# Performance work log

Hardware: AMD Instinct MI355X
Metric: run time of the kernel (lower is better)

Reference implementation:

```python
import jax, jax.numpy as jnp
import numpy as np

BS, N, DIM, HEADS = 4, 2048, 512, 8
HEAD_DIM = DIM // HEADS
SCALE = HEAD_DIM ** 0.5
NEG = -1000000.0


def setup_inputs() -> dict:
    key = jax.random.key(0)
    ks = jax.random.split(key, 6)
    x = jax.random.normal(ks[0], (BS, N, DIM), dtype=jnp.float32)
    mask = jax.random.randint(ks[1], (BS, N), 0, 2, dtype=jnp.int32)
    s = 1.0 / np.sqrt(DIM)
    Wq = jax.random.normal(ks[2], (DIM, DIM), dtype=jnp.float32) * s
    Wk = jax.random.normal(ks[3], (DIM, DIM), dtype=jnp.float32) * s
    Wv = jax.random.normal(ks[4], (DIM, DIM), dtype=jnp.float32) * s
    Wo = jax.random.normal(ks[5], (DIM, DIM), dtype=jnp.float32) * s
    return {"x": x, "Wq": Wq, "Wk": Wk, "Wv": Wv, "Wo": Wo, "mask": mask}


def reference(x, Wq, Wk, Wv, Wo, mask):
    # q,k,v: (bs, n, dim) -> (bs, h, n, d)
    def split_heads(t):
        return t.reshape(BS, N, HEADS, HEAD_DIM).transpose(0, 2, 1, 3)
    q = split_heads(x @ Wq.T)
    k = split_heads(x @ Wk.T)
    v = split_heads(x @ Wv.T)
    # scores: (bs, h, n, n)
    scores = jnp.einsum('bhqd,bhkd->bhqk', q, k) / SCALE
    # key-padding mask broadcast over heads and query positions
    keep = (mask == 1)[:, None, None, :]  # (bs,1,1,n)
    scores = jnp.where(keep, scores, NEG)
    attn = jax.nn.softmax(scores, axis=-1)
    out = jnp.einsum('bhqk,bhkd->bhqd', attn, v)
    out = out.transpose(0, 2, 1, 3).reshape(BS, N, DIM)
    return out @ Wo.T
```

## Files before the change

### kernel.cpp

```cpp
#include <hip/hip_runtime.h>
#include <hip/hip_bf16.h>

#define BS 4
#define SEQ 2048
#define DIM 512
#define HEADS 8
#define HD 64
#define ROWS (BS*SEQ)
#define SCL2E 0.1803368801111244f
#define NEGB (-1.4426950408889634e6f)

typedef __attribute__((ext_vector_type(8))) short bf16x8;
typedef __attribute__((ext_vector_type(4))) short bf16x4;
typedef __attribute__((ext_vector_type(4))) float floatx4;
typedef unsigned short u16;
typedef unsigned int u32;

#if defined(__has_builtin)
# if __has_builtin(__builtin_amdgcn_mfma_f32_16x16x16bf16_1k)
#  define HAVE_MFMA16 1
# endif
#endif
#ifndef HAVE_MFMA16
# define HAVE_MFMA16 0
#endif

__device__ __forceinline__ u16 f2bf(float f) {
    union { float f; unsigned u; } v; v.f = f;
    unsigned r = v.u + 0x7fff + ((v.u >> 16) & 1);
    return (u16)(r >> 16);
}

__device__ __forceinline__ unsigned pack2bf(float a, float b) {
#if __has_builtin(__builtin_amdgcn_cvt_pk_bf16_f32)
    typedef __attribute__((ext_vector_type(2))) __bf16 bf2;
    union { bf2 v; unsigned u; } cv;
    cv.v = __builtin_amdgcn_cvt_pk_bf16_f32(a, b);
    return cv.u;
#else
    return (unsigned)f2bf(a) | ((unsigned)f2bf(b) << 16);
#endif
}

__device__ __forceinline__ float fexp2(float x) {
#if __has_builtin(__builtin_amdgcn_exp2f)
    return __builtin_amdgcn_exp2f(x);
#else
    return __expf(x * 0.6931471805599453f);
#endif
}

__device__ __forceinline__ void gload16(const u16* g, u16* l) {
    __builtin_amdgcn_global_load_lds(
        (const __attribute__((address_space(1))) u32*)g,
        (__attribute__((address_space(3))) u32*)l, 16, 0, 0);
}

__global__ __launch_bounds__(256) void convert_all(
    const float* __restrict__ x, const float* __restrict__ Wq,
    const float* __restrict__ Wk, const float* __restrict__ Wv,
    const float* __restrict__ Wo, const int* __restrict__ mask,
    u16* __restrict__ xb, u16* __restrict__ wqb,
    u16* __restrict__ wkb, u16* __restrict__ wvb,
    u16* __restrict__ wob, float* __restrict__ biasf)
{
    int i = blockIdx.x * 256 + threadIdx.x;
    if (i < 1048576 + 262144) {
        const float* src; u16* dst; int off;
        if (i < 1048576) { src = x; dst = xb; off = i; }
        else {
            int j = i - 1048576; int seg = j >> 16; off = j & 65535;
            src = seg == 0 ? Wq : seg == 1 ? Wk : seg == 2 ? Wv : Wo;
            dst = seg == 0 ? wqb : seg == 1 ? wkb : seg == 2 ? wvb : wob;
        }
        float4 v = ((const float4*)src)[off];
        ushort4 o;
        o.x = f2bf(v.x); o.y = f2bf(v.y); o.z = f2bf(v.z); o.w = f2bf(v.w);
        ((ushort4*)dst)[off] = o;
    } else {
        int jb = i - 1310720;
        int4 mv = ((const int4*)mask)[jb];
        float4 bo;
        bo.x = (mv.x == 1) ? 0.f : NEGB;
        bo.y = (mv.y == 1) ? 0.f : NEGB;
        bo.z = (mv.z == 1) ? 0.f : NEGB;
        bo.w = (mv.w == 1) ? 0.f : NEGB;
        ((float4*)biasf)[jb] = bo;
    }
}

__global__ __launch_bounds__(256, 3) void gemm_qkv_fused(
    const u16* __restrict__ A, const u16* __restrict__ Wcat,
    u16* __restrict__ Oq, u16* __restrict__ Okf, u16* __restrict__ Ovf)
{
    __shared__ u16 ldsA[8192];
    __shared__ u16 ldsB[8192];

    int n0 = blockIdx.x * 128;
    int m0 = blockIdx.y * 128;
    int tid = threadIdx.x;
    int w = tid >> 6, lane = tid & 63, quad = lane >> 4, l16 = lane & 15;
    int mo = (w & 1) * 64, no = (w >> 1) * 64;
    int l7 = l16 & 7;

    int sr = lane >> 3, sc = lane & 7, gc = sc ^ sr;
    const u16* gA0 = A    + (long)(m0 + sr) * DIM + gc * 8;
    const u16* gB0 = Wcat + (long)(n0 + sr) * DIM + gc * 8;

    floatx4 acc[4][4];
    #pragma unroll
    for (int mt = 0; mt < 4; mt++)
        #pragma unroll
        for (int nt = 0; nt < 4; nt++) acc[mt][nt] = (floatx4){0.f,0.f,0.f,0.f};

    for (int k0 = 0; k0 < DIM; k0 += 64) {
        #pragma unroll
        for (int i = 0; i < 4; i++) {
            int ch = w * 4 + i;
            gload16(gA0 + (long)ch * 8 * DIM + k0, &ldsA[ch * 512]);
            gload16(gB0 + (long)ch * 8 * DIM + k0, &ldsB[ch * 512]);
        }
        __syncthreads();

        #pragma unroll
        for (int kc = 0; kc < 2; kc++) {
            int swz = ((kc * 4 + quad) ^ l7) * 8;
            bf16x8 af[4], bf[4];
            #pragma unroll
            for (int t4 = 0; t4 < 4; t4++) {
                af[t4] = *(const bf16x8*)&ldsA[(mo + t4*16 + l16) * 64 + swz];
                bf[t4] = *(const bf16x8*)&ldsB[(no + t4*16 + l16) * 64 + swz];
            }
            #pragma unroll
            for (int mt = 0; mt < 4; mt++)
                #pragma unroll
                for (int nt = 0; nt < 4; nt++)
                    acc[mt][nt] = __builtin_amdgcn_mfma_f32_16x16x32_bf16(
                        af[mt], bf[nt], acc[mt][nt], 0, 0, 0);
        }
        __syncthreads();
    }

    int seg = n0 >> 9;
    if (seg == 0) {
        #pragma unroll
        for (int mt = 0; mt < 4; mt++)
            #pragma unroll
            for (int nt = 0; nt < 4; nt++)
                #pragma unroll
                for (int r = 0; r < 4; r++) {
                    int row = m0 + mo + mt*16 + quad*4 + r;
                    int col9 = (n0 + no + nt*16 + l16) & 511;
                    int b = row >> 11, n = row & 2047, h = col9 >> 6, d = col9 & 63;
                    Oq[(((long)(b * HEADS + h) * SEQ + n) << 6) + d] = f2bf(acc[mt][nt][r]);
                }
    } else if (seg == 1) {
        #pragma unroll
        for (int mt = 0; mt < 4; mt++)
            #pragma unroll
            for (int nt = 0; nt < 4; nt++)
                #pragma unroll
                for (int r = 0; r < 4; r++) {
                    int row = m0 + mo + mt*16 + quad*4 + r;
                    int col9 = (n0 + no + nt*16 + l16) & 511;
                    int b = row >> 11, keyn = row & 2047, h = col9 >> 6, dd = col9 & 63;
                    int kt = keyn >> 6, ntk = (keyn >> 4) & 3, l16k = keyn & 15;
                    int g = dd >> 5, quadk = (dd >> 3) & 3, j = dd & 7;
                    long offv = ((long)((b*HEADS + h)*32 + kt) << 12)
                              + ((ntk*2 + g) << 9) + ((quadk*16 + l16k) << 3) + j;
                    Okf[offv] = f2bf(acc[mt][nt][r] * SCL2E);
                }
    } else {
#if HAVE_MFMA16
        #pragma unroll
        for (int mt = 0; mt < 4; mt++)
            #pragma unroll
            for (int nt = 0; nt < 4; nt++) {
                int rowb = m0 + mo + mt*16 + quad*4;
                int col9 = (n0 + no + nt*16 + l16) & 511;
                int b = rowb >> 11, keyn = rowb & 2047, h = col9 >> 6, dd = col9 & 63;
                int kt = keyn >> 6;
                int wf = (keyn >> 4) & 3, quadf = (keyn >> 2) & 3;
                int ctf = dd >> 4, l16f = dd & 15;
                long offv = ((long)((b*HEADS + h)*32 + kt) << 12)
                          + (wf << 10) + ((quadf*16 + l16f) << 4) + (ctf << 2);
                ushort4 st;
                st.x = f2bf(acc[mt][nt][0]); st.y = f2bf(acc[mt][nt][1]);
                st.z = f2bf(acc[mt][nt][2]); st.w = f2bf(acc[mt][nt][3]);
                *(ushort4*)&Ovf[offv] = st;
            }
#else
        #pragma unroll
        for (int mt = 0; mt < 4; mt++)
            #pragma unroll
            for (int nt = 0; nt < 4; nt++) {
                int rowb = m0 + mo + mt*16 + quad*4;
                int col9 = (n0 + no + nt*16 + l16) & 511;
                int b = rowb >> 11, keyn = rowb & 2047, h = col9 >> 6, dd = col9 & 63;
                int kt = keyn >> 6, g = (keyn >> 5) & 1, quadv = (keyn >> 3) & 3, jk = keyn & 7;
                int ctv = dd >> 4, l16v = dd & 15;
                long offv = ((long)((b*HEADS + h)*32 + kt) << 12)
                          + ((ctv*2 + g) << 9) + ((quadv*16 + l16v) << 3) + jk;
                ushort4 st;
                st.x = f2bf(acc[mt][nt][0]); st.y = f2bf(acc[mt][nt][1]);
                st.z = f2bf(acc[mt][nt][2]); st.w = f2bf(acc[mt][nt][3]);
                *(ushort4*)&Ovf[offv] = st;
            }
#endif
    }
}

#if HAVE_MFMA16
__global__ __launch_bounds__(256, 3) void flash_attn(
    const u16* __restrict__ Q, const u16* __restrict__ Kf,
    const u16* __restrict__ Vf, const float* __restrict__ biasf,
    u16* __restrict__ ctx)
{
    __shared__ float red[4352];

    int bx = blockIdx.x;
    int q0 = (bx & 31) * 64;
    int h  = (bx >> 5) & 7;
    int b  = bx >> 8;
    int bh = b * HEADS + h;

    int tid = threadIdx.x;
    int w = tid >> 6, lane = tid & 63, quad = lane >> 4, l16 = lane & 15;

    bf16x8 qb[4][2];
    #pragma unroll
    for (int nt = 0; nt < 4; nt++) {
        const u16* qp = Q + ((long)bh * SEQ + q0 + nt*16 + l16) * HD + quad * 8;
        qb[nt][0] = *(const bf16x8*)(qp);
        qb[nt][1] = *(const bf16x8*)(qp + 32);
    }

    const u16* Kbh = Kf + ((long)bh << 17) + w*1024 + lane*8;
    const u16* Vbh = Vf + ((long)bh << 17) + w*1024 + lane*16;
    const float* bb = biasf + b * SEQ + w*16 + quad*4;

    bf16x8 ka0 = *(const bf16x8*)(Kbh);
    bf16x8 ka1 = *(const bf16x8*)(Kbh + 512);
    bf16x8 vlo = *(const bf16x8*)(Vbh);
    bf16x8 vhi = *(const bf16x8*)(Vbh + 8);
    float4 bv  = *(const float4*)(bb);

    floatx4 o[4][4];
    #pragma unroll
    for (int nt = 0; nt < 4; nt++)
        #pragma unroll
        for (int ct = 0; ct < 4; ct++) o[nt][ct] = (floatx4){0.f,0.f,0.f,0.f};
    float ls[4] = {0.f, 0.f, 0.f, 0.f};

    #pragma unroll 2
    for (int t = 0; t < 32; t++) {
        bf16x8 ka0n = ka0, ka1n = ka1, vlon = vlo, vhin = vhi;
        float4 bvn = bv;
        if (t < 31) {
            const u16* kp = Kbh + (long)(t+1)*4096;
            const u16* vp = Vbh + (long)(t+1)*4096;
            ka0n = *(const bf16x8*)(kp);
            ka1n = *(const bf16x8*)(kp + 512);
            vlon = *(const bf16x8*)(vp);
            vhin = *(const bf16x8*)(vp + 8);
            bvn  = *(const float4*)(bb + (t+1)*64);
        }

        union { bf16x8 v8; bf16x4 v4[2]; } uvl, uvh;
        uvl.v8 = vlo; uvh.v8 = vhi;
        bf16x4 vb[4] = { uvl.v4[0], uvl.v4[1], uvh.v4[0], uvh.v4[1] };

        #pragma unroll
        for (int nt = 0; nt < 4; nt++) {
            floatx4 s;
            s[0] = bv.x; s[1] = bv.y; s[2] = bv.z; s[3] = bv.w;
            s = __builtin_amdgcn_mfma_f32_16x16x32_bf16(ka0, qb[nt][0], s, 0, 0, 0);
            s = __builtin_amdgcn_mfma_f32_16x16x32_bf16(ka1, qb[nt][1], s, 0, 0, 0);
            float p0 = fexp2(s[0]);
            float p1 = fexp2(s[1]);
            float p2 = fexp2(s[2]);
            float p3 = fexp2(s[3]);
            ls[nt] += (p0 + p1) + (p2 + p3);
            union { bf16x4 v; unsigned u[2]; } pu;
            pu.u[0] = pack2bf(p0, p1);
            pu.u[1] = pack2bf(p2, p3);
            #pragma unroll
            for (int ct = 0; ct < 4; ct++)
                o[nt][ct] = __builtin_amdgcn_mfma_f32_16x16x16bf16_1k(
                    pu.v, vb[ct], o[nt][ct], 0, 0, 0);
        }

        ka0 = ka0n; ka1 = ka1n; vlo = vlon; vhi = vhin; bv = bvn;
    }

    __syncthreads();
    float* ldsf = red;
    floatx4* ldsv = (floatx4*)red;

    #pragma unroll
    for (int nt = 0; nt < 4; nt++) {
        ls[nt] += __shfl_xor(ls[nt], 16);
        ls[nt] += __shfl_xor(ls[nt], 32);
    }
    if (quad == 0) {
        #pragma unroll
        for (int nt = 0; nt < 4; nt++)
            ldsf[4096 + w*64 + nt*16 + l16] = ls[nt];
    }
    __syncthreads();

    #pragma unroll
    for (int i = 1; i < 4; i++) {
        int tslot = (w + i) & 3;
        #pragma unroll
        for (int nt = 0; nt < 4; nt++)
            if (nt == tslot) {
                #pragma unroll
                for (int ct = 0; ct < 4; ct++)
                    ldsv[nt*256 + ct*64 + lane] = o[nt][ct];
            }
        __syncthreads();
        #pragma unroll
        for (int nt = 0; nt < 4; nt++)
            if (nt == w) {
                #pragma unroll
                for (int ct = 0; ct < 4; ct++) {
                    floatx4 v = ldsv[nt*256 + ct*64 + lane];
                    o[nt][ct] += v;
                }
            }
        __syncthreads();
    }

    #pragma unroll
    for (int nt = 0; nt < 4; nt++) {
        if (nt != w) continue;
        float inv[4];
        #pragma unroll
        for (int r = 0; r < 4; r++) {
            int q = w*16 + quad*4 + r;
            float s = ldsf[4096 + q] + ldsf[4096 + 64 + q]
                    + ldsf[4096 + 128 + q] + ldsf[4096 + 192 + q];
            inv[r] = 1.0f / s;
        }
        #pragma unroll
        for (int ct = 0; ct < 4; ct++) {
            int col = h * HD + ct*16 + l16;
            long rb = (long)(b * SEQ + q0 + w*16 + quad*4);
            #pragma unroll
            for (int r = 0; r < 4; r++)
                ctx[(rb + r) * DIM + col] = f2bf(o[nt][ct][r] * inv[r]);
        }
    }
}
#else
__global__ __launch_bounds__(256, 4) void flash_attn(
    const u16* __restrict__ Q, const u16* __restrict__ Kf,
    const u16* __restrict__ Vf, const float* __restrict__ biasf,
    u16* __restrict__ ctx)
{
    __shared__ u16 lds[20480];

    int bx = blockIdx.x;
    int q0 = (bx & 31) * 64;
    int h  = (bx >> 5) & 7;
    int b  = bx >> 8;
    int bh = b * HEADS + h;

    int tid = threadIdx.x;
    int w = tid >> 6, lane = tid & 63, quad = lane >> 4, l16 = lane & 15;

    const u16* Qp = Q + ((long)bh * SEQ + q0 + w*16 + l16) * HD + quad * 8;
    bf16x8 qb0 = *(const bf16x8*)(Qp);
    bf16x8 qb1 = *(const bf16x8*)(Qp + 32);

    const u16* Kbh = Kf + ((long)bh << 17);
    const u16* Vbh = Vf + ((long)bh << 17);
    const float* bbase = biasf + b * SEQ + quad * 4;

    u16* Prow = &lds[16384 + w * 1024 + l16 * 64];
    int swz = l16 & 7;

    {
        const u16* gk = Kbh + (2*w)*512 + lane*8;
        const u16* gv = Vbh + (2*w)*512 + lane*8;
        gload16(gk,       &lds[(2*w)*512]);
        gload16(gk + 512, &lds[(2*w+1)*512]);
        gload16(gv,       &lds[8192 + (2*w)*512]);
        gload16(gv + 512, &lds[8192 + (2*w+1)*512]);
    }
    __syncthreads();

    floatx4 o[4];
    #pragma unroll
    for (int ct = 0; ct < 4; ct++) o[ct] = (floatx4){0.f, 0.f, 0.f, 0.f};
    float lsum = 0.f;

    for (int t = 0; t < 32; t++) {
        int cur = t & 1;
        if (t < 31) {
            long tb = (long)(t + 1) << 12;
            int nb = cur ^ 1;
            const u16* gk = Kbh + tb + (2*w)*512 + lane*8;
            const u16* gv = Vbh + tb + (2*w)*512 + lane*8;
            gload16(gk,       &lds[nb*4096 + (2*w)*512]);
            gload16(gk + 512, &lds[nb*4096 + (2*w+1)*512]);
            gload16(gv,       &lds[8192 + nb*4096 + (2*w)*512]);
            gload16(gv + 512, &lds[8192 + nb*4096 + (2*w+1)*512]);
        }

        const u16* Kl = &lds[cur * 4096];
        const u16* Vl = &lds[8192 + cur * 4096];

        #pragma unroll
        for (int nt = 0; nt < 4; nt++) {
            float4 bv = *(const float4*)(bbase + t*64 + nt*16);
            bf16x8 ka0 = *(const bf16x8*)(Kl + (nt*2 + 0)*512 + lane*8);
            bf16x8 ka1 = *(const bf16x8*)(Kl + (nt*2 + 1)*512 + lane*8);
            floatx4 tt;
            tt[0] = bv.x; tt[1] = bv.y; tt[2] = bv.z; tt[3] = bv.w;
            tt = __builtin_amdgcn_mfma_f32_16x16x32_bf16(ka0, qb0, tt, 0, 0, 0);
            tt = __builtin_amdgcn_mfma_f32_16x16x32_bf16(ka1, qb1, tt, 0, 0, 0);
            float p0 = fexp2(tt[0]);
            float p1 = fexp2(tt[1]);
            float p2 = fexp2(tt[2]);
            float p3 = fexp2(tt[3]);
            lsum += (p0 + p1) + (p2 + p3);
            int gx = nt*2 + (quad >> 1);
            uint2 pu;
            pu.x = pack2bf(p0, p1);
            pu.y = pack2bf(p2, p3);
            *(uint2*)(Prow + ((gx ^ swz) << 3) + (quad & 1)*4) = pu;
        }

        #pragma unroll
        for (int g = 0; g < 2; g++) {
            bf16x8 pa = *(const bf16x8*)(Prow + (((g*4 + quad) ^ swz) << 3));
            #pragma unroll
            for (int ct = 0; ct < 4; ct++) {
                bf16x8 vbf = *(const bf16x8*)(Vl + (ct*2 + g)*512 + lane*8);
                o[ct] = __builtin_amdgcn_mfma_f32_16x16x32_bf16(pa, vbf, o[ct], 0, 0, 0);
            }
        }

        __syncthreads();
    }

    lsum += __shfl_xor(lsum, 16);
    lsum += __shfl_xor(lsum, 32);
    float inv = 1.0f / lsum;
    float i0 = __shfl(inv, quad*4 + 0);
    float i1 = __shfl(inv, quad*4 + 1);
    float i2 = __shfl(inv, quad*4 + 2);
    float i3 = __shfl(inv, quad*4 + 3);
    #pragma unroll
    for (int ct = 0; ct < 4; ct++) {
        int col = h * HD + ct*16 + l16;
        long rb = (long)(b * SEQ + q0 + w*16 + quad*4);
        ctx[(rb + 0) * DIM + col] = f2bf(o[ct][0] * i0);
        ctx[(rb + 1) * DIM + col] = f2bf(o[ct][1] * i1);
        ctx[(rb + 2) * DIM + col] = f2bf(o[ct][2] * i2);
        ctx[(rb + 3) * DIM + col] = f2bf(o[ct][3] * i3);
    }
}
#endif

__global__ __launch_bounds__(256, 4) void gemm_proj(
    const u16* __restrict__ A, const u16* __restrict__ Bt,
    float* __restrict__ Out)
{
    __shared__ u16 ldsA[4096];
    __shared__ u16 ldsB[8192];

    int n0 = blockIdx.x * 128;
    int m0 = blockIdx.y * 64;
    int tid = threadIdx.x;
    int w = tid >> 6, lane = tid & 63, quad = lane >> 4, l16 = lane & 15;
    int l7 = l16 & 7;

    int sr = lane >> 3, sc = lane & 7, gc = sc ^ sr;
    const u16* gA0 = A  + (long)(m0 + sr) * DIM + gc * 8;
    const u16* gB0 = Bt + (long)(n0 + sr) * DIM + gc * 8;

    floatx4 acc[8];
    #pragma unroll
    for (int nt = 0; nt < 8; nt++) acc[nt] = (floatx4){0.f,0.f,0.f,0.f};

    for (int k0 = 0; k0 < DIM; k0 += 64) {
        gload16(gA0 + (long)(2*w)   * 8 * DIM + k0, &ldsA[(2*w)   * 512]);
        gload16(gA0 + (long)(2*w+1) * 8 * DIM + k0, &ldsA[(2*w+1) * 512]);
        #pragma unroll
        for (int i = 0; i < 4; i++)
            gload16(gB0 + (long)(4*w+i) * 8 * DIM + k0, &ldsB[(4*w+i) * 512]);
        __syncthreads();

        #pragma unroll
        for (int kc = 0; kc < 2; kc++) {
            int swz = ((kc * 4 + quad) ^ l7) * 8;
            bf16x8 af = *(const bf16x8*)&ldsA[(w*16 + l16) * 64 + swz];
            #pragma unroll
            for (int nt = 0; nt < 8; nt++) {
                bf16x8 bfv = *(const bf16x8*)&ldsB[(nt*16 + l16) * 64 + swz];
                acc[nt] = __builtin_amdgcn_mfma_f32_16x16x32_bf16(
                    af, bfv, acc[nt], 0, 0, 0);
            }
        }
        __syncthreads();
    }

    #pragma unroll
    for (int nt = 0; nt < 8; nt++)
        #pragma unroll
        for (int r = 0; r < 4; r++) {
            int row = m0 + w*16 + quad*4 + r;
            int col = n0 + nt*16 + l16;
            Out[(long)row * DIM + col] = acc[nt][r];
        }
}

extern "C" void kernel_launch(void* const* d_in, const int* in_sizes, int n_in,
                              void* d_out, int out_size, void* d_ws, size_t ws_size,
                              hipStream_t stream) {
    const float* x  = (const float*)d_in[0];
    const float* Wq = (const float*)d_in[1];
    const float* Wk = (const float*)d_in[2];
    const float* Wv = (const float*)d_in[3];
    const float* Wo = (const float*)d_in[4];
    const int* mask = (const int*)d_in[5];
    float* out = (float*)d_out;

    char* ws = (char*)d_ws;
    size_t off = 0;
    u16* xb  = (u16*)(ws + off); off += (size_t)ROWS * DIM * 2;
    u16* wqb = (u16*)(ws + off); off += (size_t)DIM * DIM * 2;
    u16* wkb = (u16*)(ws + off); off += (size_t)DIM * DIM * 2;
    u16* wvb = (u16*)(ws + off); off += (size_t)DIM * DIM * 2;
    u16* wob = (u16*)(ws + off); off += (size_t)DIM * DIM * 2;
    u16* Qh  = (u16*)(ws + off); off += (size_t)ROWS * DIM * 2;
    u16* Kfr = (u16*)(ws + off); off += (size_t)ROWS * DIM * 2;
    u16* Vfr = (u16*)(ws + off); off += (size_t)ROWS * DIM * 2;
    u16* ctx = (u16*)(ws + off); off += (size_t)ROWS * DIM * 2;
    float* biasf = (float*)(ws + off); off += (size_t)BS * SEQ * 4;

    convert_all<<<5128, 256, 0, stream>>>(x, Wq, Wk, Wv, Wo, mask,
                                          xb, wqb, wkb, wvb, wob, biasf);
    gemm_qkv_fused<<<dim3(12, 64), 256, 0, stream>>>(xb, wqb, Qh, Kfr, Vfr);
    flash_attn<<<BS * HEADS * (SEQ / 64), 256, 0, stream>>>(Qh, Kfr, Vfr, biasf, ctx);
    gemm_proj<<<dim3(4, 128), 256, 0, stream>>>(ctx, wob, out);

    (void)in_sizes; (void)n_in; (void)out_size; (void)ws_size;
}
```

Baseline: 164.3 us.

## Compute softmax denominators via extra MFMA with ones vector and remap block order

Drops the per-thread VALU accumulation of exponentials and the cross-lane shuffle reduction. The row sums are now produced by one extra MFMA per tile that multiplies the probability fragment by a ones column. The block index mapping also changes so that consecutive blocks cover different batch-head pairs rather than consecutive query tiles of one head, which alters cache locality for K/V. The cost is one more MFMA per tile and four more accumulator registers, which could raise register pressure under launch_bounds(256,3).

```diff
diff --git a/kernel.cpp b/kernel.cpp
--- a/kernel.cpp
+++ b/kernel.cpp
@@ -219,9 +219,12 @@
     __shared__ float red[4352];
 
     int bx = blockIdx.x;
-    int q0 = (bx & 31) * 64;
-    int h  = (bx >> 5) & 7;
-    int b  = bx >> 8;
+    int c  = bx & 7, s = bx >> 3;
+    int g  = ((s >> 5) << 3) | c;
+    int i  = s & 31;
+    int q0 = i * 64;
+    int h  = g & 7;
+    int b  = g >> 3;
     int bh = b * HEADS + h;
 
     int tid = threadIdx.x;
@@ -238,6 +241,9 @@
     const u16* Kbh = Kf + ((long)bh << 17) + w*1024 + lane*8;
     const u16* Vbh = Vf + ((long)bh << 17) + w*1024 + lane*16;
     const float* bb = biasf + b * SEQ + w*16 + quad*4;
+
+    short one_s = (l16 == 0) ? (short)0x3F80 : (short)0;
+    bf16x4 onesb = { one_s, one_s, one_s, one_s };
 
     bf16x8 ka0 = *(const bf16x8*)(Kbh);
     bf16x8 ka1 = *(const bf16x8*)(Kbh + 512);
@@ -246,11 +252,13 @@
     float4 bv  = *(const float4*)(bb);
 
     floatx4 o[4][4];
-    #pragma unroll
-    for (int nt = 0; nt < 4; nt++)
+    floatx4 o5[4];
+    #pragma unroll
+    for (int nt = 0; nt < 4; nt++) {
         #pragma unroll
         for (int ct = 0; ct < 4; ct++) o[nt][ct] = (floatx4){0.f,0.f,0.f,0.f};
-    float ls[4] = {0.f, 0.f, 0.f, 0.f};
+        o5[nt] = (floatx4){0.f,0.f,0.f,0.f};
+    }
 
     #pragma unroll 2
     for (int t = 0; t < 32; t++) {
@@ -272,15 +280,14 @@
 
         #pragma unroll
         for (int nt = 0; nt < 4; nt++) {
-            floatx4 s;
-            s[0] = bv.x; s[1] = bv.y; s[2] = bv.z; s[3] = bv.w;
-            s = __builtin_amdgcn_mfma_f32_16x16x32_bf16(ka0, qb[nt][0], s, 0, 0, 0);
-            s = __builtin_amdgcn_mfma_f32_16x16x32_bf16(ka1, qb[nt][1], s, 0, 0, 0);
-            float p0 = fexp2(s[0]);
-            float p1 = fexp2(s[1]);
-            float p2 = fexp2(s[2]);
-            float p3 = fexp2(s[3]);
-            ls[nt] += (p0 + p1) + (p2 + p3);
+            floatx4 s2;
+            s2[0] = bv.x; s2[1] = bv.y; s2[2] = bv.z; s2[3] = bv.w;
+            s2 = __builtin_amdgcn_mfma_f32_16x16x32_bf16(ka0, qb[nt][0], s2, 0, 0, 0);
+            s2 = __builtin_amdgcn_mfma_f32_16x16x32_bf16(ka1, qb[nt][1], s2, 0, 0, 0);
+            float p0 = fexp2(s2[0]);
+            float p1 = fexp2(s2[1]);
+            float p2 = fexp2(s2[2]);
+            float p3 = fexp2(s2[3]);
             union { bf16x4 v; unsigned u[2]; } pu;
             pu.u[0] = pack2bf(p0, p1);
             pu.u[1] = pack2bf(p2, p3);
@@ -288,6 +295,8 @@
             for (int ct = 0; ct < 4; ct++)
                 o[nt][ct] = __builtin_amdgcn_mfma_f32_16x16x16bf16_1k(
                     pu.v, vb[ct], o[nt][ct], 0, 0, 0);
+            o5[nt] = __builtin_amdgcn_mfma_f32_16x16x16bf16_1k(
+                pu.v, onesb, o5[nt], 0, 0, 0);
         }
 
         ka0 = ka0n; ka1 = ka1n; vlo = vlon; vhi = vhin; bv = bvn;
@@ -297,21 +306,18 @@
     float* ldsf = red;
     floatx4* ldsv = (floatx4*)red;
 
-    #pragma unroll
-    for (int nt = 0; nt < 4; nt++) {
-        ls[nt] += __shfl_xor(ls[nt], 16);
-        ls[nt] += __shfl_xor(ls[nt], 32);
-    }
-    if (quad == 0) {
+    if (l16 == 0) {
         #pragma unroll
         for (int nt = 0; nt < 4; nt++)
-            ldsf[4096 + w*64 + nt*16 + l16] = ls[nt];
+            #pragma unroll
+            for (int r = 0; r < 4; r++)
+                ldsf[4096 + w*64 + nt*16 + quad*4 + r] = o5[nt][r];
     }
     __syncthreads();
 
     #pragma unroll
-    for (int i = 1; i < 4; i++) {
-        int tslot = (w + i) & 3;
+    for (int i2 = 1; i2 < 4; i2++) {
+        int tslot = (w + i2) & 3;
         #pragma unroll
         for (int nt = 0; nt < 4; nt++)
             if (nt == tslot) {
@@ -339,9 +345,9 @@
         #pragma unroll
         for (int r = 0; r < 4; r++) {
             int q = w*16 + quad*4 + r;
-            float s = ldsf[4096 + q] + ldsf[4096 + 64 + q]
-                    + ldsf[4096 + 128 + q] + ldsf[4096 + 192 + q];
-            inv[r] = 1.0f / s;
+            float sden = ldsf[4096 + q] + ldsf[4096 + 64 + q]
+                       + ldsf[4096 + 128 + q] + ldsf[4096 + 192 + q];
+            inv[r] = 1.0f / sden;
         }
         #pragma unroll
         for (int ct = 0; ct < 4; ct++) {
```

Result: faster. 156.6 us (-4.7%).
